# Optimization experiments

Measured on AMD Instinct MI355X. Metric: run time of the kernel, lower is better.

The kernel has to match this reference:

```python
import jax, jax.numpy as jnp
import numpy as np

N, C, D = 64, 4, 2048
K = 64          # kernel_size (shapelet length)
O = 256         # out_channels (number of shapelets)
L = D - K + 1   # number of sliding windows


def setup_inputs() -> dict:
    key = jax.random.key(0)
    k1, k2 = jax.random.split(key)
    x_input = jax.random.normal(k1, (N, C, D), dtype=jnp.float32)
    weight = jax.random.normal(k2, (O, C, K), dtype=jnp.float32)
    return {"x_input": x_input, "weight": weight}


def reference(x_input, weight):
    # im2col: sliding windows of length K -> (n, c, L, K)
    idx = jnp.arange(L)[:, None] + jnp.arange(K)[None, :]  # (L, K)
    windows = x_input[:, :, idx]                            # (n, c, L, K)
    # pairwise squared distances per channel, normalized by K
    x_norm = jnp.sum(windows * windows, axis=-1)            # (n, c, L)
    y_norm = jnp.sum(weight * weight, axis=-1)              # (o, c)
    cross = jnp.einsum('nclk,ock->ncol', windows, weight)   # (n, c, o, L)
    dist = (x_norm[:, :, None, :] + y_norm.T[None, :, :, None] - 2.0 * cross)
    dist = jnp.maximum(dist, 0.0) / K                       # clamp(., 0, inf) / len
    return dist  # (n, in_channels, out_channels, L)
```

## Files before the change

### kernel.cpp

```cpp
#include <hip/hip_runtime.h>

#define N_ 64
#define C_ 4
#define D_ 2048
#define K_ 64
#define O_ 256
#define L_ 1985
#define XPAD 2112
#define XCOPY 2116
#define OPITCH 2020
#define NTILE 125

typedef __attribute__((ext_vector_type(8))) short s16x8;
typedef __attribute__((ext_vector_type(4))) float f32x4;
typedef __attribute__((ext_vector_type(4), aligned(4))) float f32x4u;

#define BAR_LGKM() do { \
    asm volatile("s_waitcnt lgkmcnt(0)\n\ts_barrier" ::: "memory"); \
    __builtin_amdgcn_sched_barrier(0); \
} while (0)

__device__ __forceinline__ unsigned short f2bf(float f) {
    union { float f; unsigned u; } v; v.f = f;
    unsigned u = v.u;
    u += 0x7fffu + ((u >> 16) & 1u);
    return (unsigned short)(u >> 16);
}

__global__ __launch_bounds__(256) void prep_w(const float* __restrict__ w,
                                              unsigned short* __restrict__ wb,
                                              float* __restrict__ yn) {
    int o = blockIdx.x;
    int tid = threadIdx.x;
    int c = tid >> 6, k = tid & 63;
    size_t idx = (size_t)(o * C_ + c) * K_ + k;
    float v = w[idx];
    wb[idx] = f2bf(v);
    float s = v * v;
    for (int off = 32; off > 0; off >>= 1) s += __shfl_down(s, off, 64);
    if (k == 0) yn[o * C_ + c] = s;
}

__global__ __launch_bounds__(1024) void shapelet_main(const float* __restrict__ x,
                                                      const unsigned short* __restrict__ wb,
                                                      const float* __restrict__ yn,
                                                      float* __restrict__ out) {
    __shared__ __align__(16) unsigned short xs[4][XCOPY];
    __shared__ float xn[D_];
    __shared__ __align__(16) float ost[16 * OPITCH];

    int nc = blockIdx.x;
    int c = nc & (C_ - 1);
    const float* xrow = x + (size_t)nc * D_;
    int tid = threadIdx.x;

    for (int i = tid; i < XPAD; i += 1024) ost[i] = (i < D_) ? xrow[i] : 0.f;
    __syncthreads();
    for (int i = tid; i < XCOPY; i += 1024) {
        #pragma unroll
        for (int s = 0; s < 4; ++s) {
            int idx = i + s;
            xs[s][i] = (idx < XPAD) ? f2bf(ost[idx]) : (unsigned short)0;
        }
    }
    for (int l = tid; l < D_; l += 1024) {
        float ssum = 0.f;
        #pragma unroll 16
        for (int k = 0; k < K_; ++k) { float v = ost[l + k]; ssum = fmaf(v, v, ssum); }
        xn[l] = ssum;
    }
    __syncthreads();

    int wave = tid >> 6, lane = tid & 63, lr = lane & 15, hi = lane >> 4;
    const unsigned short* xbase = &xs[lr & 3][(lr & ~3) + hi * 8];
    int dj = lane;

    for (int st = 0; st < 16; ++st) {
        int o = st * 16 + lr;
        s16x8 wfr[2];
        #pragma unroll
        for (int kk = 0; kk < 2; ++kk)
            wfr[kk] = *reinterpret_cast<const s16x8*>(
                wb + ((size_t)o * C_ + c) * K_ + kk * 32 + hi * 8);
        float ynv = yn[o * C_ + c];

        for (int t = wave; t < NTILE; t += 16) {
            int l0t = t * 16;
            f32x4 acc = {0.f, 0.f, 0.f, 0.f};
            #pragma unroll
            for (int kk = 0; kk < 2; ++kk) {
                const unsigned long long* p =
                    (const unsigned long long*)(xbase + l0t + kk * 32);
                union { unsigned long long u[2]; s16x8 v; } a;
                a.u[0] = p[0]; a.u[1] = p[1];
                acc = __builtin_amdgcn_mfma_f32_16x16x32_bf16(a.v, wfr[kk], acc, 0, 0, 0);
            }
            f32x4 xv = *reinterpret_cast<const f32x4*>(&xn[l0t + hi * 4]);
            f32x4 r;
            #pragma unroll
            for (int j = 0; j < 4; ++j)
                r[j] = fmaxf(xv[j] + ynv - 2.f * acc[j], 0.f) * (1.f / (float)K_);
            *reinterpret_cast<f32x4*>(&ost[lr * OPITCH + l0t + hi * 4]) = r;
        }
        BAR_LGKM();

        float* gb = out + ((size_t)nc * O_ + st * 16 + wave) * L_;
        const float* src = &ost[wave * OPITCH];
        for (int pos = dj * 4; pos + 4 <= L_; pos += 256) {
            f32x4 v = *reinterpret_cast<const f32x4*>(src + pos);
            __builtin_nontemporal_store(v, (f32x4u*)(gb + pos));
        }
        if (dj == 0) __builtin_nontemporal_store(src[L_ - 1], gb + (L_ - 1));
        BAR_LGKM();
    }
}

extern "C" void kernel_launch(void* const* d_in, const int* in_sizes, int n_in,
                              void* d_out, int out_size, void* d_ws, size_t ws_size,
                              hipStream_t stream) {
    const float* x = (const float*)d_in[0];
    const float* w = (const float*)d_in[1];
    float* out = (float*)d_out;

    unsigned short* wb = (unsigned short*)d_ws;
    float* yn = (float*)((char*)d_ws + (size_t)O_ * C_ * K_ * 2);

    prep_w<<<O_, 256, 0, stream>>>(w, wb, yn);
    shapelet_main<<<N_ * C_, 1024, 0, stream>>>(x, wb, yn, out);
}
```

Before: 131.8 us.

## Use prefix sums for window norms, fold 1/K scaling, unroll tile and store loops

Result: faster. 121.3 us (-7.9%).

```diff
diff --git a/kernel.cpp b/kernel.cpp
--- a/kernel.cpp
+++ b/kernel.cpp
@@ -6,14 +6,12 @@
 #define K_ 64
 #define O_ 256
 #define L_ 1985
-#define XPAD 2112
 #define XCOPY 2116
 #define OPITCH 2020
 #define NTILE 125
 
 typedef __attribute__((ext_vector_type(8))) short s16x8;
 typedef __attribute__((ext_vector_type(4))) float f32x4;
-typedef __attribute__((ext_vector_type(4), aligned(4))) float f32x4u;
 
 #define BAR_LGKM() do { \
     asm volatile("s_waitcnt lgkmcnt(0)\n\ts_barrier" ::: "memory"); \
@@ -29,7 +27,7 @@
 
 __global__ __launch_bounds__(256) void prep_w(const float* __restrict__ w,
                                               unsigned short* __restrict__ wb,
-                                              float* __restrict__ yn) {
+                                              float* __restrict__ ynK) {
     int o = blockIdx.x;
     int tid = threadIdx.x;
     int c = tid >> 6, k = tid & 63;
@@ -38,12 +36,12 @@
     wb[idx] = f2bf(v);
     float s = v * v;
     for (int off = 32; off > 0; off >>= 1) s += __shfl_down(s, off, 64);
-    if (k == 0) yn[o * C_ + c] = s;
+    if (k == 0) ynK[o * C_ + c] = s * 0.015625f;
 }
 
 __global__ __launch_bounds__(1024) void shapelet_main(const float* __restrict__ x,
                                                       const unsigned short* __restrict__ wb,
-                                                      const float* __restrict__ yn,
+                                                      const float* __restrict__ ynK,
                                                       float* __restrict__ out) {
     __shared__ __align__(16) unsigned short xs[4][XCOPY];
     __shared__ float xn[D_];
@@ -54,20 +52,31 @@
     const float* xrow = x + (size_t)nc * D_;
     int tid = threadIdx.x;
 
-    for (int i = tid; i < XPAD; i += 1024) ost[i] = (i < D_) ? xrow[i] : 0.f;
+    float* z    = ost;
+    float* pre  = ost + 2176;
+    float* S16v = ost + 2176 + 2112;
+
+    for (int i = tid; i < 2112; i += 1024) {
+        float v = (i < D_) ? xrow[i] : 0.f;
+        z[i] = v * v;
+        unsigned short b = f2bf(v);
+        #pragma unroll
+        for (int s = 0; s < 4; ++s) { int j = i - s; if (j >= 0) xs[s][j] = b; }
+    }
     __syncthreads();
-    for (int i = tid; i < XCOPY; i += 1024) {
+    if (tid < 132) {
+        float run = 0.f;
+        int base = tid * 16;
         #pragma unroll
-        for (int s = 0; s < 4; ++s) {
-            int idx = i + s;
-            xs[s][i] = (idx < XPAD) ? f2bf(ost[idx]) : (unsigned short)0;
-        }
+        for (int j = 0; j < 16; ++j) { pre[base + j] = run; run += z[base + j]; }
+        S16v[tid] = run;
     }
+    __syncthreads();
     for (int l = tid; l < D_; l += 1024) {
-        float ssum = 0.f;
-        #pragma unroll 16
-        for (int k = 0; k < K_; ++k) { float v = ost[l + k]; ssum = fmaf(v, v, ssum); }
-        xn[l] = ssum;
+        int a = l >> 4, b = l & 15;
+        float s = S16v[a] - pre[a * 16 + b] + S16v[a + 1] + S16v[a + 2]
+                + S16v[a + 3] + pre[(a + 4) * 16 + b];
+        xn[l] = s * 0.015625f;
     }
     __syncthreads();
 
@@ -77,40 +86,46 @@
 
     for (int st = 0; st < 16; ++st) {
         int o = st * 16 + lr;
-        s16x8 wfr[2];
+        const s16x8* wp = reinterpret_cast<const s16x8*>(
+            wb + ((size_t)o * C_ + c) * K_ + hi * 8);
+        s16x8 w0 = wp[0];
+        s16x8 w1 = wp[4];
+        float ynKv = ynK[o * C_ + c];
+
         #pragma unroll
-        for (int kk = 0; kk < 2; ++kk)
-            wfr[kk] = *reinterpret_cast<const s16x8*>(
-                wb + ((size_t)o * C_ + c) * K_ + kk * 32 + hi * 8);
-        float ynv = yn[o * C_ + c];
-
-        for (int t = wave; t < NTILE; t += 16) {
-            int l0t = t * 16;
+        for (int i = 0; i < 8; ++i) {
+            int t = wave + i * 16;
+            int tc = t > 124 ? 124 : t;
+            int l0t = tc * 16;
+            union { unsigned long long u[2]; s16x8 v; } a0, a1;
+            const unsigned long long* p0 = (const unsigned long long*)(xbase + l0t);
+            a0.u[0] = p0[0]; a0.u[1] = p0[1];
+            const unsigned long long* p1 = (const unsigned long long*)(xbase + l0t + 32);
+            a1.u[0] = p1[0]; a1.u[1] = p1[1];
             f32x4 acc = {0.f, 0.f, 0.f, 0.f};
-            #pragma unroll
-            for (int kk = 0; kk < 2; ++kk) {
-                const unsigned long long* p =
-                    (const unsigned long long*)(xbase + l0t + kk * 32);
-                union { unsigned long long u[2]; s16x8 v; } a;
-                a.u[0] = p[0]; a.u[1] = p[1];
-                acc = __builtin_amdgcn_mfma_f32_16x16x32_bf16(a.v, wfr[kk], acc, 0, 0, 0);
-            }
+            acc = __builtin_amdgcn_mfma_f32_16x16x32_bf16(a0.v, w0, acc, 0, 0, 0);
+            acc = __builtin_amdgcn_mfma_f32_16x16x32_bf16(a1.v, w1, acc, 0, 0, 0);
             f32x4 xv = *reinterpret_cast<const f32x4*>(&xn[l0t + hi * 4]);
             f32x4 r;
             #pragma unroll
             for (int j = 0; j < 4; ++j)
-                r[j] = fmaxf(xv[j] + ynv - 2.f * acc[j], 0.f) * (1.f / (float)K_);
-            *reinterpret_cast<f32x4*>(&ost[lr * OPITCH + l0t + hi * 4]) = r;
+                r[j] = fmaxf(fmaf(acc[j], -0.03125f, xv[j] + ynKv), 0.f);
+            if (t < NTILE)
+                *reinterpret_cast<f32x4*>(&ost[lr * OPITCH + l0t + hi * 4]) = r;
         }
         BAR_LGKM();
 
         float* gb = out + ((size_t)nc * O_ + st * 16 + wave) * L_;
         const float* src = &ost[wave * OPITCH];
-        for (int pos = dj * 4; pos + 4 <= L_; pos += 256) {
-            f32x4 v = *reinterpret_cast<const f32x4*>(src + pos);
-            __builtin_nontemporal_store(v, (f32x4u*)(gb + pos));
+        #pragma unroll
+        for (int q = 0; q < 8; ++q) {
+            int pos = dj * 4 + q * 256;
+            if (pos + 4 <= L_) {
+                f32x4 v = *reinterpret_cast<const f32x4*>(src + pos);
+                __builtin_memcpy(gb + pos, &v, 16);
+            }
         }
-        if (dj == 0) __builtin_nontemporal_store(src[L_ - 1], gb + (L_ - 1));
+        if (dj == 0) gb[L_ - 1] = src[L_ - 1];
         BAR_LGKM();
     }
 }
@@ -123,8 +138,8 @@
     float* out = (float*)d_out;
 
     unsigned short* wb = (unsigned short*)d_ws;
-    float* yn = (float*)((char*)d_ws + (size_t)O_ * C_ * K_ * 2);
+    float* ynK = (float*)((char*)d_ws + (size_t)O_ * C_ * K_ * 2);
 
-    prep_w<<<O_, 256, 0, stream>>>(w, wb, yn);
-    shapelet_main<<<N_ * C_, 1024, 0, stream>>>(x, wb, yn, out);
+    prep_w<<<O_, 256, 0, stream>>>(w, wb, ynK);
+    shapelet_main<<<N_ * C_, 1024, 0, stream>>>(x, wb, ynK, out);
 }
```
